# Performance work log

Hardware: AMD Instinct MI355X
Metric: run time of the kernel (lower is better)

## Reference

```python
import jax, jax.numpy as jnp
import numpy as np

N = 50000
E = 800000
IN = 256
HID = 64
H12 = 4
LAT = 32
NEG_SLOPE = 0.2


def gat_conv(x, src, dst, W, a_src, a_dst, b, heads, out_ch, concat):
    """PyG GATConv (eval mode, add_self_loops already applied to src/dst).
    x: [N, F_in]; src/dst: [Etot]; W: [F_in, heads*out_ch]; a_*: [heads, out_ch]; b: bias.
    Returns (out, alpha[Etot, heads])."""
    n = x.shape[0]
    h = (x @ W).reshape(n, heads, out_ch)                 # [N,H,C]
    e_src = (h * a_src).sum(-1)                           # [N,H]
    e_dst = (h * a_dst).sum(-1)                           # [N,H]
    e = jax.nn.leaky_relu(e_src[src] + e_dst[dst], NEG_SLOPE)   # [Etot,H]
    emax = jax.ops.segment_max(e, dst, num_segments=n)
    ee = jnp.exp(e - emax[dst])
    denom = jax.ops.segment_sum(ee, dst, num_segments=n)
    alpha = ee / (denom[dst] + 1e-16)                     # segment softmax over incoming edges
    msg = h[src] * alpha[:, :, None]                      # [Etot,H,C]
    out = jax.ops.segment_sum(msg, dst, num_segments=n)   # [N,H,C]
    out = out.reshape(n, heads * out_ch) if concat else out.mean(axis=1)
    return out + b, alpha


def setup_inputs() -> dict:
    key = jax.random.key(0)
    ks = jax.random.split(key, 20)
    s = 0.1
    inp = {
        "x": jax.random.normal(ks[0], (N, IN), jnp.float32),
        "edge_index": jax.random.randint(ks[1], (2, E), 0, N, jnp.int32),
        "W1": jax.random.normal(ks[2], (IN, H12 * HID), jnp.float32) * s,
        "a1s": jax.random.normal(ks[3], (H12, HID), jnp.float32) * s,
        "a1d": jax.random.normal(ks[4], (H12, HID), jnp.float32) * s,
        "b1": jnp.zeros((H12 * HID,), jnp.float32),
        "W2": jax.random.normal(ks[5], (H12 * HID, H12 * HID), jnp.float32) * s,
        "a2s": jax.random.normal(ks[6], (H12, HID), jnp.float32) * s,
        "a2d": jax.random.normal(ks[7], (H12, HID), jnp.float32) * s,
        "b2": jnp.zeros((HID,), jnp.float32),
        "Wm": jax.random.normal(ks[8], (HID, LAT), jnp.float32) * s,
        "ams": jax.random.normal(ks[9], (1, LAT), jnp.float32) * s,
        "amd": jax.random.normal(ks[10], (1, LAT), jnp.float32) * s,
        "bm": jnp.zeros((LAT,), jnp.float32),
        # log_std head
        "Ws": jax.random.normal(ks[11], (HID, LAT), jnp.float32) * s,
        "ass": jax.random.normal(ks[12], (1, LAT), jnp.float32) * s,
        "asd": jax.random.normal(ks[13], (1, LAT), jnp.float32) * s,
        "bs": jnp.zeros((LAT,), jnp.float32),
    }
    return inp


def reference(x, edge_index, W1, a1s, a1d, b1, W2, a2s, a2d, b2,
              Wm, ams, amd, bm, Ws, ass, asd, bs):
    # GATConv adds self loops by default
    loops = jnp.arange(N, dtype=edge_index.dtype)
    src = jnp.concatenate([edge_index[0], loops])
    dst = jnp.concatenate([edge_index[1], loops])

    h1, a_w1 = gat_conv(x, src, dst, W1, a1s, a1d, b1, H12, HID, True)
    h1 = jax.nn.relu(h1)
    h2, a_w2 = gat_conv(h1, src, dst, W2, a2s, a2d, b2, H12, HID, False)
    h2 = jax.nn.relu(h2)  # dropout is identity in eval mode
    z_mean, a_wm = gat_conv(h2, src, dst, Wm, ams, amd, bm, 1, LAT, False)
    z_log_std, a_ws = gat_conv(h2, src, dst, Ws, ass, asd, bs, 1, LAT, False)
    return (z_mean, z_log_std, a_w1, a_w2, a_wm, a_ws)
```

## Files before the change

### kernel.cpp

```cpp
#include <hip/hip_runtime.h>
#include <cstdint>
#include <cstddef>

#define NN 50000
#define EE 800000
#define ETOT 850000
#define NEG_SLOPE 0.2f

typedef _Float16 f16;
typedef __attribute__((ext_vector_type(8))) _Float16 f16x8;
typedef __attribute__((ext_vector_type(4))) float f32x4;


__global__ __launch_bounds__(256) void deg_kernel(const int* __restrict__ ei, int* __restrict__ deg) {
    int e = blockIdx.x * 256 + threadIdx.x;
    if (e >= ETOT) return;
    int d = (e < EE) ? ei[EE + e] : (e - EE);
    atomicAdd(&deg[d], 1);
}

__global__ __launch_bounds__(256) void scan1_kernel(const int* __restrict__ deg, int* __restrict__ offs,
                                                    int* __restrict__ bsum, int n) {
    __shared__ int sh[256];
    int i = blockIdx.x * 256 + threadIdx.x;
    int v = (i < n) ? deg[i] : 0;
    sh[threadIdx.x] = v;
    __syncthreads();
    for (int off = 1; off < 256; off <<= 1) {
        int t = (threadIdx.x >= off) ? sh[threadIdx.x - off] : 0;
        __syncthreads();
        sh[threadIdx.x] += t;
        __syncthreads();
    }
    if (i < n) offs[i] = sh[threadIdx.x] - v;
    if (threadIdx.x == 255) bsum[blockIdx.x] = sh[255];
}

__global__ __launch_bounds__(256) void scan2_kernel(int* __restrict__ bsum, int nb) {
    __shared__ int sh[256];
    int v = (threadIdx.x < nb) ? bsum[threadIdx.x] : 0;
    sh[threadIdx.x] = v;
    __syncthreads();
    for (int off = 1; off < 256; off <<= 1) {
        int t = (threadIdx.x >= off) ? sh[threadIdx.x - off] : 0;
        __syncthreads();
        sh[threadIdx.x] += t;
        __syncthreads();
    }
    if (threadIdx.x < nb) bsum[threadIdx.x] = sh[threadIdx.x] - v;
}

__global__ __launch_bounds__(256) void scan3_kernel(const int* __restrict__ bsum, int* __restrict__ offs,
                                                    int* __restrict__ cursor, int n) {
    int i = blockIdx.x * 256 + threadIdx.x;
    if (i < n) {
        int o = offs[i] + bsum[blockIdx.x];
        offs[i] = o;
        cursor[i] = o;
    }
}

__global__ __launch_bounds__(256) void fill_kernel(const int* __restrict__ ei, int* __restrict__ cursor,
                                                   int* __restrict__ csrc) {
    int e = blockIdx.x * 256 + threadIdx.x;
    if (e >= ETOT) return;
    int d, s;
    if (e < EE) { s = ei[e]; d = ei[EE + e]; } else { s = e - EE; d = e - EE; }
    int p = atomicAdd(&cursor[d], 1);
    csrc[p] = s;
}

__device__ __forceinline__ float leaky(float v) { return v > 0.f ? v : NEG_SLOPE * v; }


template<int K, int NH, bool AF32, int ALPHA_NH>
__global__ __launch_bounds__(256) void mfma_gemm_fused(
    const void* __restrict__ Ap, const f16* __restrict__ Bt, f16* __restrict__ C,
    const float* __restrict__ aS, const float* __restrict__ aD,
    float* __restrict__ es, float* __restrict__ edi, int M, int N, int RB,
    const int* __restrict__ ei, const float* __restrict__ esA,
    const float* __restrict__ ediA, float* __restrict__ awA) {
    if ((int)blockIdx.y >= RB) {
        if constexpr (ALPHA_NH == 4) {
            int e = (((int)blockIdx.y - RB) * (int)gridDim.x + (int)blockIdx.x) * 256 + (int)threadIdx.x;
            if (e >= ETOT) return;
            int s, d;
            if (e < EE) { s = ei[e]; d = ei[EE + e]; } else { s = e - EE; d = e - EE; }
            float4 esv = *(const float4*)(esA + (size_t)s * 4);
            float4 edv = *(const float4*)(ediA + (size_t)d * 8);
            float4 iv  = *(const float4*)(ediA + (size_t)d * 8 + 4);
            float4 r;
            r.x = __expf(leaky(esv.x + edv.x)) * iv.x;
            r.y = __expf(leaky(esv.y + edv.y)) * iv.y;
            r.z = __expf(leaky(esv.z + edv.z)) * iv.z;
            r.w = __expf(leaky(esv.w + edv.w)) * iv.w;
            *(float4*)(awA + (size_t)e * 4) = r;
        }
        return;
    }
    int w = threadIdx.x >> 6, lane = threadIdx.x & 63;
    int m0 = blockIdx.y * 128 + w * 32;
    int n0 = blockIdx.x * 64;
    int r = lane & 15, kb = lane >> 4;
    int ar0 = m0 + r;       if (ar0 > M - 1) ar0 = M - 1;
    int ar1 = m0 + 16 + r;  if (ar1 > M - 1) ar1 = M - 1;
    f32x4 acc[2][4] = {};
    const float* Af = (const float*)Ap;
    const f16*   Ah = (const f16*)Ap;
    size_t a0off = (size_t)ar0 * K + kb * 8;
    size_t a1off = (size_t)ar1 * K + kb * 8;
    const f16* bbase = Bt + (size_t)(n0 + r) * K + kb * 8;
    for (int k0 = 0; k0 < K; k0 += 32) {
        f16x8 a0, a1;
        if constexpr (AF32) {
            float4 l0 = *(const float4*)(Af + a0off + k0);
            float4 h0 = *(const float4*)(Af + a0off + k0 + 4);
            float4 l1 = *(const float4*)(Af + a1off + k0);
            float4 h1 = *(const float4*)(Af + a1off + k0 + 4);
            a0[0]=(f16)l0.x; a0[1]=(f16)l0.y; a0[2]=(f16)l0.z; a0[3]=(f16)l0.w;
            a0[4]=(f16)h0.x; a0[5]=(f16)h0.y; a0[6]=(f16)h0.z; a0[7]=(f16)h0.w;
            a1[0]=(f16)l1.x; a1[1]=(f16)l1.y; a1[2]=(f16)l1.z; a1[3]=(f16)l1.w;
            a1[4]=(f16)h1.x; a1[5]=(f16)h1.y; a1[6]=(f16)h1.z; a1[7]=(f16)h1.w;
        } else {
            a0 = *(const f16x8*)(Ah + a0off + k0);
            a1 = *(const f16x8*)(Ah + a1off + k0);
        }
#pragma unroll
        for (int ni = 0; ni < 4; ++ni) {
            f16x8 b = *(const f16x8*)(bbase + (size_t)ni * 16 * K + k0);
            acc[0][ni] = __builtin_amdgcn_mfma_f32_16x16x32_f16(a0, b, acc[0][ni], 0, 0, 0);
            acc[1][ni] = __builtin_amdgcn_mfma_f32_16x16x32_f16(a1, b, acc[1][ni], 0, 0, 0);
        }
    }
    float aSl[4], aDl[4];
#pragma unroll
    for (int ni = 0; ni < 4; ++ni) {
        aSl[ni] = aS[n0 + ni * 16 + r];
        aDl[ni] = aD[n0 + ni * 16 + r];
    }
#pragma unroll
    for (int mi = 0; mi < 2; ++mi) {
#pragma unroll
        for (int i = 0; i < 4; ++i) {
            int row = m0 + mi * 16 + kb * 4 + i;
            bool ok = row < M;
            if (ok) {
#pragma unroll
                for (int ni = 0; ni < 4; ++ni)
                    C[(size_t)row * N + n0 + ni * 16 + r] = (f16)acc[mi][ni][i];
            }
            if constexpr (NH == 4) {
                float pes = acc[mi][0][i] * aSl[0] + acc[mi][1][i] * aSl[1] + acc[mi][2][i] * aSl[2] + acc[mi][3][i] * aSl[3];
                float ped = acc[mi][0][i] * aDl[0] + acc[mi][1][i] * aDl[1] + acc[mi][2][i] * aDl[2] + acc[mi][3][i] * aDl[3];
#pragma unroll
                for (int off = 1; off < 16; off <<= 1) {
                    pes += __shfl_xor(pes, off);
                    ped += __shfl_xor(ped, off);
                }
                if (r == 0 && ok) {
                    es[(size_t)row * 4 + blockIdx.x] = pes;
                    edi[(size_t)row * 8 + blockIdx.x] = ped;
                }
            } else {
                float p0s = acc[mi][0][i] * aSl[0] + acc[mi][1][i] * aSl[1];
                float p1s = acc[mi][2][i] * aSl[2] + acc[mi][3][i] * aSl[3];
                float p0d = acc[mi][0][i] * aDl[0] + acc[mi][1][i] * aDl[1];
                float p1d = acc[mi][2][i] * aDl[2] + acc[mi][3][i] * aDl[3];
#pragma unroll
                for (int off = 1; off < 16; off <<= 1) {
                    p0s += __shfl_xor(p0s, off);
                    p1s += __shfl_xor(p1s, off);
                    p0d += __shfl_xor(p0d, off);
                    p1d += __shfl_xor(p1d, off);
                }
                if (r == 0 && ok) {
                    es[(size_t)row * 2 + 0] = p0s;
                    es[(size_t)row * 2 + 1] = p1s;
                    edi[(size_t)row * 4 + 0] = p0d;
                    edi[(size_t)row * 4 + 1] = p1d;
                }
            }
        }
    }
}


__global__ __launch_bounds__(256) void packw_kernel(const float* __restrict__ W1, const float* __restrict__ W2,
                                                    const float* __restrict__ Wm, const float* __restrict__ Ws,
                                                    const float* __restrict__ ams, const float* __restrict__ ass,
                                                    const float* __restrict__ amd, const float* __restrict__ asd,
                                                    f16* __restrict__ Wt1, f16* __restrict__ Wt2,
                                                    f16* __restrict__ Wtms,
                                                    float* __restrict__ aS, float* __restrict__ aD) {
    int i = blockIdx.x * 256 + threadIdx.x;
    if (i < 65536) {
        int n = i >> 8, k = i & 255;
        Wt1[(size_t)n * 256 + k] = (f16)W1[(size_t)k * 256 + n];
        Wt2[(size_t)n * 256 + k] = (f16)W2[(size_t)k * 256 + n];
    }
    if (i < 4096) {
        int c = i >> 6, k = i & 63;
        float v = (c < 32) ? Wm[k * 32 + c] : Ws[k * 32 + (c - 32)];
        Wtms[(size_t)c * 64 + k] = (f16)v;
    }
    if (i < 64) {
        aS[i] = (i < 32) ? ams[i] : ass[i - 32];
        aD[i] = (i < 32) ? amd[i] : asd[i - 32];
    }
}


__global__ __launch_bounds__(256) void alpha_ms_kernel(const int* __restrict__ ei, const float* __restrict__ es,
                                                       const float* __restrict__ edi,
                                                       float* __restrict__ awm, float* __restrict__ aws) {
    int e = blockIdx.x * 256 + threadIdx.x;
    if (e >= ETOT) return;
    int s, d;
    if (e < EE) { s = ei[e]; d = ei[EE + e]; } else { s = e - EE; d = e - EE; }
    float2 esv = *(const float2*)(es + (size_t)s * 2);
    float2 edv = *(const float2*)(edi + (size_t)d * 4);
    float2 iv  = *(const float2*)(edi + (size_t)d * 4 + 2);
    awm[e] = __expf(leaky(esv.x + edv.x)) * iv.x;
    aws[e] = __expf(leaky(esv.y + edv.y)) * iv.y;
}


__global__ __launch_bounds__(64) void agg_concat_kernel(
    const f16* __restrict__ H, const float* __restrict__ es, float* __restrict__ edi,
    const int* __restrict__ offs, const int* __restrict__ csrc,
    const float* __restrict__ bias, f16* __restrict__ out) {
    int lane = threadIdx.x;
    int n = blockIdx.x;
    int start = offs[n];
    int end = (n + 1 < NN) ? offs[n + 1] : ETOT;
    int deg = end - start;
    int h16 = lane >> 4, sub = lane & 15;
    float edh = edi[(size_t)n * 8 + h16];
    float dsum = 0.f;
    for (int j = sub; j < deg; j += 16) {
        int s = csrc[start + j];
        dsum += __expf(leaky(es[s * 4 + h16] + edh));
    }
    for (int off = 1; off < 16; off <<= 1) dsum += __shfl_xor(dsum, off);
    float inv = 1.f / (dsum + 1e-16f);
    if (sub == 0) edi[(size_t)n * 8 + 4 + h16] = inv;
    int half = lane >> 5;
    int l5 = lane & 31;
    int hh = l5 >> 3;
    int c8 = l5 * 8;
    float invh = __shfl(inv, hh << 4);
    float edhh = __shfl(edh, hh << 4);
    float accv[8] = {};
    int j = half;
    for (; j + 6 < deg; j += 8) {
        int p0 = start + j, p1 = start + j + 2, p2 = start + j + 4, p3 = start + j + 6;
        int s0 = csrc[p0], s1 = csrc[p1], s2 = csrc[p2], s3 = csrc[p3];
        float a0 = __expf(leaky(es[s0 * 4 + hh] + edhh)) * invh;
        float a1 = __expf(leaky(es[s1 * 4 + hh] + edhh)) * invh;
        float a2 = __expf(leaky(es[s2 * 4 + hh] + edhh)) * invh;
        float a3 = __expf(leaky(es[s3 * 4 + hh] + edhh)) * invh;
        f16x8 v0 = *(const f16x8*)(H + (size_t)s0 * 256 + c8);
        f16x8 v1 = *(const f16x8*)(H + (size_t)s1 * 256 + c8);
        f16x8 v2 = *(const f16x8*)(H + (size_t)s2 * 256 + c8);
        f16x8 v3 = *(const f16x8*)(H + (size_t)s3 * 256 + c8);
#pragma unroll
        for (int k = 0; k < 8; ++k)
            accv[k] += a0 * (float)v0[k] + a1 * (float)v1[k] + a2 * (float)v2[k] + a3 * (float)v3[k];
    }
    for (; j < deg; j += 2) {
        int s0 = csrc[start + j];
        float a0 = __expf(leaky(es[s0 * 4 + hh] + edhh)) * invh;
        f16x8 v0 = *(const f16x8*)(H + (size_t)s0 * 256 + c8);
#pragma unroll
        for (int k = 0; k < 8; ++k) accv[k] += a0 * (float)v0[k];
    }
#pragma unroll
    for (int k = 0; k < 8; ++k) accv[k] += __shfl_xor(accv[k], 32);
    if (lane < 32) {
        f16x8 r;
#pragma unroll
        for (int k = 0; k < 8; ++k) r[k] = (f16)fmaxf(accv[k] + bias[c8 + k], 0.f);
        *(f16x8*)(out + (size_t)n * 256 + c8) = r;
    }
}


__global__ __launch_bounds__(64) void agg_mean_kernel(
    const f16* __restrict__ H, const float* __restrict__ es, float* __restrict__ edi,
    const int* __restrict__ offs, const int* __restrict__ csrc,
    const float* __restrict__ bias, f16* __restrict__ out) {
    int lane = threadIdx.x;
    int n = blockIdx.x;
    int start = offs[n];
    int end = (n + 1 < NN) ? offs[n + 1] : ETOT;
    int deg = end - start;
    int h16 = lane >> 4, sub = lane & 15;
    float edh = edi[(size_t)n * 8 + h16];
    float dsum = 0.f;
    for (int j = sub; j < deg; j += 16) {
        int s = csrc[start + j];
        dsum += __expf(leaky(es[s * 4 + h16] + edh));
    }
    for (int off = 1; off < 16; off <<= 1) dsum += __shfl_xor(dsum, off);
    float inv = 1.f / (dsum + 1e-16f);
    if (sub == 0) edi[(size_t)n * 8 + 4 + h16] = inv;
    int half = lane >> 5;
    int l5 = lane & 31;
    int hh = l5 >> 3;
    int c8 = l5 * 8;
    float invh = __shfl(inv, hh << 4);
    float edhh = __shfl(edh, hh << 4);
    float accv[8] = {};
    int j = half;
    for (; j + 6 < deg; j += 8) {
        int p0 = start + j, p1 = start + j + 2, p2 = start + j + 4, p3 = start + j + 6;
        int s0 = csrc[p0], s1 = csrc[p1], s2 = csrc[p2], s3 = csrc[p3];
        float a0 = __expf(leaky(es[s0 * 4 + hh] + edhh)) * invh;
        float a1 = __expf(leaky(es[s1 * 4 + hh] + edhh)) * invh;
        float a2 = __expf(leaky(es[s2 * 4 + hh] + edhh)) * invh;
        float a3 = __expf(leaky(es[s3 * 4 + hh] + edhh)) * invh;
        f16x8 v0 = *(const f16x8*)(H + (size_t)s0 * 256 + c8);
        f16x8 v1 = *(const f16x8*)(H + (size_t)s1 * 256 + c8);
        f16x8 v2 = *(const f16x8*)(H + (size_t)s2 * 256 + c8);
        f16x8 v3 = *(const f16x8*)(H + (size_t)s3 * 256 + c8);
#pragma unroll
        for (int k = 0; k < 8; ++k)
            accv[k] += a0 * (float)v0[k] + a1 * (float)v1[k] + a2 * (float)v2[k] + a3 * (float)v3[k];
    }
    for (; j < deg; j += 2) {
        int s0 = csrc[start + j];
        float a0 = __expf(leaky(es[s0 * 4 + hh] + edhh)) * invh;
        f16x8 v0 = *(const f16x8*)(H + (size_t)s0 * 256 + c8);
#pragma unroll
        for (int k = 0; k < 8; ++k) accv[k] += a0 * (float)v0[k];
    }
#pragma unroll
    for (int k = 0; k < 8; ++k) {
        accv[k] += __shfl_xor(accv[k], 8);
        accv[k] += __shfl_xor(accv[k], 16);
        accv[k] += __shfl_xor(accv[k], 32);
    }
    if (lane < 8) {
        f16x8 r;
#pragma unroll
        for (int k = 0; k < 8; ++k) r[k] = (f16)fmaxf(accv[k] * 0.25f + bias[lane * 8 + k], 0.f);
        *(f16x8*)(out + (size_t)n * 64 + lane * 8) = r;
    }
}


__global__ __launch_bounds__(64) void agg_ms_kernel(
    const f16* __restrict__ H, const float* __restrict__ es, float* __restrict__ edi,
    const int* __restrict__ offs, const int* __restrict__ csrc,
    const float* __restrict__ bm, const float* __restrict__ bs,
    float* __restrict__ zmean, float* __restrict__ zlog) {
    int lane = threadIdx.x;
    int n = blockIdx.x;
    int start = offs[n];
    int end = (n + 1 < NN) ? offs[n + 1] : ETOT;
    int deg = end - start;
    int g = lane >> 5, sub = lane & 31;
    float edg = edi[(size_t)n * 4 + g];
    float dsum = 0.f;
    for (int j = sub; j < deg; j += 32) {
        int s = csrc[start + j];
        dsum += __expf(leaky(es[s * 2 + g] + edg));
    }
    for (int off = 1; off < 32; off <<= 1) dsum += __shfl_xor(dsum, off);
    float inv = 1.f / (dsum + 1e-16f);
    if (sub == 0) edi[(size_t)n * 4 + 2 + g] = inv;
    int slot = lane >> 3;
    int le = lane & 7;
    int g2 = le >> 2;
    int c8 = le * 8;
    float invg = __shfl(inv, g2 << 5);
    float edg2 = __shfl(edg, g2 << 5);
    float accv[8] = {};
    for (int j = slot; j < deg; j += 8) {
        int p = start + j;
        int s = csrc[p];
        float a = __expf(leaky(es[s * 2 + g2] + edg2)) * invg;
        f16x8 v = *(const f16x8*)(H + (size_t)s * 64 + c8);
#pragma unroll
        for (int k = 0; k < 8; ++k) accv[k] += a * (float)v[k];
    }
#pragma unroll
    for (int k = 0; k < 8; ++k) {
        accv[k] += __shfl_xor(accv[k], 8);
        accv[k] += __shfl_xor(accv[k], 16);
        accv[k] += __shfl_xor(accv[k], 32);
    }
    if (lane < 4) {
        float4 r0, r1;
        int cb = lane * 8;
        r0.x = accv[0] + bm[cb + 0]; r0.y = accv[1] + bm[cb + 1];
        r0.z = accv[2] + bm[cb + 2]; r0.w = accv[3] + bm[cb + 3];
        r1.x = accv[4] + bm[cb + 4]; r1.y = accv[5] + bm[cb + 5];
        r1.z = accv[6] + bm[cb + 6]; r1.w = accv[7] + bm[cb + 7];
        *(float4*)(zmean + (size_t)n * 32 + cb) = r0;
        *(float4*)(zmean + (size_t)n * 32 + cb + 4) = r1;
    } else if (lane < 8) {
        float4 r0, r1;
        int cb = (lane - 4) * 8;
        r0.x = accv[0] + bs[cb + 0]; r0.y = accv[1] + bs[cb + 1];
        r0.z = accv[2] + bs[cb + 2]; r0.w = accv[3] + bs[cb + 3];
        r1.x = accv[4] + bs[cb + 4]; r1.y = accv[5] + bs[cb + 5];
        r1.z = accv[6] + bs[cb + 6]; r1.w = accv[7] + bs[cb + 7];
        *(float4*)(zlog + (size_t)n * 32 + cb) = r0;
        *(float4*)(zlog + (size_t)n * 32 + cb + 4) = r1;
    }
}


extern "C" void kernel_launch(void* const* d_in, const int* in_sizes, int n_in,
                              void* d_out, int out_size, void* d_ws, size_t ws_size,
                              hipStream_t stream) {
    const float* x   = (const float*)d_in[0];
    const int*   ei  = (const int*)d_in[1];
    const float* W1  = (const float*)d_in[2];
    const float* a1s = (const float*)d_in[3];
    const float* a1d = (const float*)d_in[4];
    const float* b1  = (const float*)d_in[5];
    const float* W2  = (const float*)d_in[6];
    const float* a2s = (const float*)d_in[7];
    const float* a2d = (const float*)d_in[8];
    const float* b2  = (const float*)d_in[9];
    const float* Wm  = (const float*)d_in[10];
    const float* ams = (const float*)d_in[11];
    const float* amd = (const float*)d_in[12];
    const float* bm  = (const float*)d_in[13];
    const float* Ws  = (const float*)d_in[14];
    const float* ass = (const float*)d_in[15];
    const float* asd = (const float*)d_in[16];
    const float* bs  = (const float*)d_in[17];

    float* out = (float*)d_out;
    float* zmean = out;
    float* zlog  = out + 1600000;
    float* a_w1  = out + 3200000;
    float* a_w2  = out + 6600000;
    float* a_wm  = out + 10000000;
    float* a_ws_o = out + 10850000;

    float* ws = (float*)d_ws;
    size_t o = 0;
    f16*   Hh   = (f16*)(ws + o); o += (size_t)NN * 128;
    f16*   h1h  = (f16*)(ws + o); o += (size_t)NN * 128;
    f16*   h2h  = (f16*)(ws + o); o += (size_t)NN * 32;
    float* es1  = ws + o; o += NN * 4;
    float* es2  = ws + o; o += NN * 4;
    float* esms = ws + o; o += NN * 2;
    float* edi1 = ws + o; o += NN * 8;
    float* edi2 = ws + o; o += NN * 8;
    float* edims= ws + o; o += NN * 4;
    f16*   Wt1  = (f16*)(ws + o); o += 32768;
    f16*   Wt2  = (f16*)(ws + o); o += 32768;
    f16*   Wtms = (f16*)(ws + o); o += 2048;
    float* aSms = ws + o; o += 64;
    float* aDms = ws + o; o += 64;
    int* deg    = (int*)(ws + o); o += NN;
    int* offs   = (int*)(ws + o); o += NN;
    int* cursor = (int*)(ws + o); o += NN;
    int* csrc   = (int*)(ws + o); o += ETOT;

    const int edgeBlocks = (ETOT + 255) / 256;
    const int nodeBlocks = (NN + 255) / 256;
    const int RB = (NN + 127) / 128;

    hipMemsetAsync(deg, 0, NN * sizeof(int), stream);
    deg_kernel<<<edgeBlocks, 256, 0, stream>>>(ei, deg);
    scan1_kernel<<<nodeBlocks, 256, 0, stream>>>(deg, offs, cursor , NN);
    scan2_kernel<<<1, 256, 0, stream>>>(cursor, nodeBlocks);
    scan3_kernel<<<nodeBlocks, 256, 0, stream>>>(cursor, offs, deg , NN);
    fill_kernel<<<edgeBlocks, 256, 0, stream>>>(ei, deg, csrc);

    packw_kernel<<<256, 256, 0, stream>>>(W1, W2, Wm, Ws, ams, ass, amd, asd, Wt1, Wt2, Wtms, aSms, aDms);

    dim3 gg1(4, RB);
    dim3 gg2(4, RB + (edgeBlocks + 3) / 4);
    dim3 gg3(1, RB + edgeBlocks);

    mfma_gemm_fused<256, 4, true, 0><<<gg1, 256, 0, stream>>>(
        x, Wt1, Hh, a1s, a1d, es1, edi1, NN, 256, RB, nullptr, nullptr, nullptr, nullptr);
    agg_concat_kernel<<<NN, 64, 0, stream>>>(Hh, es1, edi1, offs, csrc, b1, h1h);

    mfma_gemm_fused<256, 4, false, 4><<<gg2, 256, 0, stream>>>(
        h1h, Wt2, Hh, a2s, a2d, es2, edi2, NN, 256, RB, ei, es1, edi1, a_w1);
    agg_mean_kernel<<<NN, 64, 0, stream>>>(Hh, es2, edi2, offs, csrc, b2, h2h);

    mfma_gemm_fused<64, 2, false, 4><<<gg3, 256, 0, stream>>>(
        h2h, Wtms, Hh, aSms, aDms, esms, edims, NN, 64, RB, ei, es2, edi2, a_w2);
    agg_ms_kernel<<<NN, 64, 0, stream>>>(Hh, esms, edims, offs, csrc, bm, bs, zmean, zlog);

    alpha_ms_kernel<<<edgeBlocks, 256, 0, stream>>>(ei, esms, edims, a_wm, a_ws_o);
}
```

Baseline: 511.8 us.

## Fuse CSR build into weight packing, single-block scan, and layer-1 GEMM tail

Merges the degree-count atomics into the weight-packing kernel and replaces the three-kernel scan with one 1024-thread scan block. The CSR fill (atomic cursor scatter) now runs as extra tail blocks of the first GEMM launch instead of a separate kernel. This cuts the number of small kernel launches and lets the fill overlap with the GEMM. The cost is a serial single-block scan over 50k nodes and more register or scheduling pressure in the fused GEMM.

```diff
diff --git a/kernel.cpp b/kernel.cpp
--- a/kernel.cpp
+++ b/kernel.cpp
@@ -11,81 +11,91 @@
 typedef __attribute__((ext_vector_type(8))) _Float16 f16x8;
 typedef __attribute__((ext_vector_type(4))) float f32x4;
 
-
-__global__ __launch_bounds__(256) void deg_kernel(const int* __restrict__ ei, int* __restrict__ deg) {
-    int e = blockIdx.x * 256 + threadIdx.x;
-    if (e >= ETOT) return;
-    int d = (e < EE) ? ei[EE + e] : (e - EE);
-    atomicAdd(&deg[d], 1);
-}
-
-__global__ __launch_bounds__(256) void scan1_kernel(const int* __restrict__ deg, int* __restrict__ offs,
-                                                    int* __restrict__ bsum, int n) {
-    __shared__ int sh[256];
-    int i = blockIdx.x * 256 + threadIdx.x;
-    int v = (i < n) ? deg[i] : 0;
-    sh[threadIdx.x] = v;
+__device__ __forceinline__ float leaky(float v) { return v > 0.f ? v : NEG_SLOPE * v; }
+
+
+__global__ __launch_bounds__(1024) void scan_one_kernel(const int* __restrict__ deg, int* __restrict__ offs,
+                                                        int* __restrict__ cursor, int n) {
+    __shared__ int sh[1024];
+    int tid = threadIdx.x;
+    int per = (n + 1023) / 1024;
+    int base = tid * per;
+    int sum = 0;
+    for (int i = 0; i < per; ++i) {
+        int idx = base + i;
+        if (idx < n) sum += deg[idx];
+    }
+    sh[tid] = sum;
     __syncthreads();
-    for (int off = 1; off < 256; off <<= 1) {
-        int t = (threadIdx.x >= off) ? sh[threadIdx.x - off] : 0;
+    for (int off = 1; off < 1024; off <<= 1) {
+        int t = (tid >= off) ? sh[tid - off] : 0;
         __syncthreads();
-        sh[threadIdx.x] += t;
+        sh[tid] += t;
         __syncthreads();
     }
-    if (i < n) offs[i] = sh[threadIdx.x] - v;
-    if (threadIdx.x == 255) bsum[blockIdx.x] = sh[255];
-}
-
-__global__ __launch_bounds__(256) void scan2_kernel(int* __restrict__ bsum, int nb) {
-    __shared__ int sh[256];
-    int v = (threadIdx.x < nb) ? bsum[threadIdx.x] : 0;
-    sh[threadIdx.x] = v;
-    __syncthreads();
-    for (int off = 1; off < 256; off <<= 1) {
-        int t = (threadIdx.x >= off) ? sh[threadIdx.x - off] : 0;
-        __syncthreads();
-        sh[threadIdx.x] += t;
-        __syncthreads();
-    }
-    if (threadIdx.x < nb) bsum[threadIdx.x] = sh[threadIdx.x] - v;
-}
-
-__global__ __launch_bounds__(256) void scan3_kernel(const int* __restrict__ bsum, int* __restrict__ offs,
-                                                    int* __restrict__ cursor, int n) {
-    int i = blockIdx.x * 256 + threadIdx.x;
-    if (i < n) {
-        int o = offs[i] + bsum[blockIdx.x];
-        offs[i] = o;
-        cursor[i] = o;
-    }
-}
-
-__global__ __launch_bounds__(256) void fill_kernel(const int* __restrict__ ei, int* __restrict__ cursor,
-                                                   int* __restrict__ csrc) {
-    int e = blockIdx.x * 256 + threadIdx.x;
-    if (e >= ETOT) return;
-    int d, s;
-    if (e < EE) { s = ei[e]; d = ei[EE + e]; } else { s = e - EE; d = e - EE; }
-    int p = atomicAdd(&cursor[d], 1);
-    csrc[p] = s;
-}
-
-__device__ __forceinline__ float leaky(float v) { return v > 0.f ? v : NEG_SLOPE * v; }
-
-
-template<int K, int NH, bool AF32, int ALPHA_NH>
+    int run = sh[tid] - sum;
+    for (int i = 0; i < per; ++i) {
+        int idx = base + i;
+        if (idx < n) {
+            offs[idx] = run;
+            cursor[idx] = run;
+            run += deg[idx];
+        }
+    }
+}
+
+
+__global__ __launch_bounds__(256) void packw_deg_kernel(
+    const float* __restrict__ W1, const float* __restrict__ W2,
+    const float* __restrict__ Wm, const float* __restrict__ Ws,
+    const float* __restrict__ ams, const float* __restrict__ ass,
+    const float* __restrict__ amd, const float* __restrict__ asd,
+    f16* __restrict__ Wt1, f16* __restrict__ Wt2, f16* __restrict__ Wtms,
+    float* __restrict__ aS, float* __restrict__ aD,
+    const int* __restrict__ ei, int* __restrict__ deg) {
+    int b = blockIdx.x;
+    if (b >= 256) {
+        int e = (b - 256) * 256 + threadIdx.x;
+        if (e >= ETOT) return;
+        int d = (e < EE) ? ei[EE + e] : (e - EE);
+        atomicAdd(&deg[d], 1);
+        return;
+    }
+    int i = b * 256 + threadIdx.x;
+    {
+        int n = i >> 8, k = i & 255;
+        Wt1[(size_t)n * 256 + k] = (f16)W1[(size_t)k * 256 + n];
+        Wt2[(size_t)n * 256 + k] = (f16)W2[(size_t)k * 256 + n];
+    }
+    if (i < 4096) {
+        int c = i >> 6, k = i & 63;
+        float v = (c < 32) ? Wm[k * 32 + c] : Ws[k * 32 + (c - 32)];
+        Wtms[(size_t)c * 64 + k] = (f16)v;
+    }
+    if (i < 64) {
+        aS[i] = (i < 32) ? ams[i] : ass[i - 32];
+        aD[i] = (i < 32) ? amd[i] : asd[i - 32];
+    }
+}
+
+
+template<int K, int NH, bool AF32, int TAILMODE>
 __global__ __launch_bounds__(256) void mfma_gemm_fused(
     const void* __restrict__ Ap, const f16* __restrict__ Bt, f16* __restrict__ C,
     const float* __restrict__ aS, const float* __restrict__ aD,
     float* __restrict__ es, float* __restrict__ edi, int M, int N, int RB,
     const int* __restrict__ ei, const float* __restrict__ esA,
-    const float* __restrict__ ediA, float* __restrict__ awA) {
+    const float* __restrict__ ediA, float* __restrict__ awA,
+    int* __restrict__ tcur, int* __restrict__ tcsrc) {
     if ((int)blockIdx.y >= RB) {
-        if constexpr (ALPHA_NH == 4) {
-            int e = (((int)blockIdx.y - RB) * (int)gridDim.x + (int)blockIdx.x) * 256 + (int)threadIdx.x;
-            if (e >= ETOT) return;
-            int s, d;
-            if (e < EE) { s = ei[e]; d = ei[EE + e]; } else { s = e - EE; d = e - EE; }
+        int e = (((int)blockIdx.y - RB) * (int)gridDim.x + (int)blockIdx.x) * 256 + (int)threadIdx.x;
+        if (e >= ETOT) return;
+        int s, d;
+        if (e < EE) { s = ei[e]; d = ei[EE + e]; } else { s = e - EE; d = e - EE; }
+        if constexpr (TAILMODE == 1) {
+            int p = atomicAdd(&tcur[d], 1);
+            tcsrc[p] = s;
+        } else if constexpr (TAILMODE == 2) {
             float4 esv = *(const float4*)(esA + (size_t)s * 4);
             float4 edv = *(const float4*)(ediA + (size_t)d * 8);
             float4 iv  = *(const float4*)(ediA + (size_t)d * 8 + 4);
@@ -185,31 +195,6 @@
 }
 
 
-__global__ __launch_bounds__(256) void packw_kernel(const float* __restrict__ W1, const float* __restrict__ W2,
-                                                    const float* __restrict__ Wm, const float* __restrict__ Ws,
-                                                    const float* __restrict__ ams, const float* __restrict__ ass,
-                                                    const float* __restrict__ amd, const float* __restrict__ asd,
-                                                    f16* __restrict__ Wt1, f16* __restrict__ Wt2,
-                                                    f16* __restrict__ Wtms,
-                                                    float* __restrict__ aS, float* __restrict__ aD) {
-    int i = blockIdx.x * 256 + threadIdx.x;
-    if (i < 65536) {
-        int n = i >> 8, k = i & 255;
-        Wt1[(size_t)n * 256 + k] = (f16)W1[(size_t)k * 256 + n];
-        Wt2[(size_t)n * 256 + k] = (f16)W2[(size_t)k * 256 + n];
-    }
-    if (i < 4096) {
-        int c = i >> 6, k = i & 63;
-        float v = (c < 32) ? Wm[k * 32 + c] : Ws[k * 32 + (c - 32)];
-        Wtms[(size_t)c * 64 + k] = (f16)v;
-    }
-    if (i < 64) {
-        aS[i] = (i < 32) ? ams[i] : ass[i - 32];
-        aD[i] = (i < 32) ? amd[i] : asd[i - 32];
-    }
-}
-
-
 __global__ __launch_bounds__(256) void alpha_ms_kernel(const int* __restrict__ ei, const float* __restrict__ es,
                                                        const float* __restrict__ edi,
                                                        float* __restrict__ awm, float* __restrict__ aws) {
@@ -464,32 +449,29 @@
     int* csrc   = (int*)(ws + o); o += ETOT;
 
     const int edgeBlocks = (ETOT + 255) / 256;
-    const int nodeBlocks = (NN + 255) / 256;
     const int RB = (NN + 127) / 128;
+    const int tailY4 = (edgeBlocks + 3) / 4;
 
     hipMemsetAsync(deg, 0, NN * sizeof(int), stream);
-    deg_kernel<<<edgeBlocks, 256, 0, stream>>>(ei, deg);
-    scan1_kernel<<<nodeBlocks, 256, 0, stream>>>(deg, offs, cursor , NN);
-    scan2_kernel<<<1, 256, 0, stream>>>(cursor, nodeBlocks);
-    scan3_kernel<<<nodeBlocks, 256, 0, stream>>>(cursor, offs, deg , NN);
-    fill_kernel<<<edgeBlocks, 256, 0, stream>>>(ei, deg, csrc);
-
-    packw_kernel<<<256, 256, 0, stream>>>(W1, W2, Wm, Ws, ams, ass, amd, asd, Wt1, Wt2, Wtms, aSms, aDms);
-
-    dim3 gg1(4, RB);
-    dim3 gg2(4, RB + (edgeBlocks + 3) / 4);
+    packw_deg_kernel<<<256 + edgeBlocks, 256, 0, stream>>>(
+        W1, W2, Wm, Ws, ams, ass, amd, asd, Wt1, Wt2, Wtms, aSms, aDms, ei, deg);
+
+    scan_one_kernel<<<1, 1024, 0, stream>>>(deg, offs, cursor, NN);
+
+    dim3 gg1(4, RB + tailY4);
+    dim3 gg2(4, RB + tailY4);
     dim3 gg3(1, RB + edgeBlocks);
 
-    mfma_gemm_fused<256, 4, true, 0><<<gg1, 256, 0, stream>>>(
-        x, Wt1, Hh, a1s, a1d, es1, edi1, NN, 256, RB, nullptr, nullptr, nullptr, nullptr);
+    mfma_gemm_fused<256, 4, true, 1><<<gg1, 256, 0, stream>>>(
+        x, Wt1, Hh, a1s, a1d, es1, edi1, NN, 256, RB, ei, nullptr, nullptr, nullptr, cursor, csrc);
     agg_concat_kernel<<<NN, 64, 0, stream>>>(Hh, es1, edi1, offs, csrc, b1, h1h);
 
-    mfma_gemm_fused<256, 4, false, 4><<<gg2, 256, 0, stream>>>(
-        h1h, Wt2, Hh, a2s, a2d, es2, edi2, NN, 256, RB, ei, es1, edi1, a_w1);
+    mfma_gemm_fused<256, 4, false, 2><<<gg2, 256, 0, stream>>>(
+        h1h, Wt2, Hh, a2s, a2d, es2, edi2, NN, 256, RB, ei, es1, edi1, a_w1, nullptr, nullptr);
     agg_mean_kernel<<<NN, 64, 0, stream>>>(Hh, es2, edi2, offs, csrc, b2, h2h);
 
-    mfma_gemm_fused<64, 2, false, 4><<<gg3, 256, 0, stream>>>(
-        h2h, Wtms, Hh, aSms, aDms, esms, edims, NN, 64, RB, ei, es2, edi2, a_w2);
+    mfma_gemm_fused<64, 2, false, 2><<<gg3, 256, 0, stream>>>(
+        h2h, Wtms, Hh, aSms, aDms, esms, edims, NN, 64, RB, ei, es2, edi2, a_w2, nullptr, nullptr);
     agg_ms_kernel<<<NN, 64, 0, stream>>>(Hh, esms, edims, offs, csrc, bm, bs, zmean, zlog);
 
     alpha_ms_kernel<<<edgeBlocks, 256, 0, stream>>>(ei, esms, edims, a_wm, a_ws_o);
```

Result: slower. 596.0 us (+16.5%).
